# Performance work log

Measured on AMD Instinct MI355X. Metric: run time of the kernel, lower is better.

Reference implementation:

```python
import jax, jax.numpy as jnp
import numpy as np

INPUT_DIM = 1024
EMBED_DIM = 1024
NUM_HEADS = 16
HEAD_DIM = EMBED_DIM // NUM_HEADS


def _xavier_uniform(key, shape):
    fan_in, fan_out = shape[1], shape[0]
    limit = float(np.sqrt(6.0 / (fan_in + fan_out)))
    return jax.random.uniform(key, shape, jnp.float32, -limit, limit)


def setup_inputs() -> dict:
    key = jax.random.key(0)
    kx, kqkv, ko = jax.random.split(key, 3)
    x = jax.random.normal(kx, (2, 2048, INPUT_DIM), jnp.float32)
    # torch Linear stores weight as [out, in]; we keep that convention
    w_qkv = _xavier_uniform(kqkv, (3 * EMBED_DIM, INPUT_DIM))
    b_qkv = jnp.zeros((3 * EMBED_DIM,), jnp.float32)
    w_o = _xavier_uniform(ko, (EMBED_DIM, EMBED_DIM))
    b_o = jnp.zeros((EMBED_DIM,), jnp.float32)
    return {"x": x, "w_qkv": w_qkv, "b_qkv": b_qkv, "w_o": w_o, "b_o": b_o}


def reference(x, w_qkv, b_qkv, w_o, b_o):
    B, S, _ = x.shape
    H, D = NUM_HEADS, HEAD_DIM
    qkv = jnp.einsum("bsi,oi->bso", x, w_qkv) + b_qkv          # [B,S,3E]
    qkv = qkv.reshape(B, S, H, 3 * D).transpose(0, 2, 1, 3)    # [B,H,S,3D]
    q, k, v = jnp.split(qkv, 3, axis=-1)                        # each [B,H,S,D]
    scores = jnp.einsum("bhqd,bhkd->bhqk", q, k) / jnp.sqrt(jnp.float32(D))
    attn = jax.nn.softmax(scores, axis=-1)                      # [B,H,S,S]
    vals = jnp.einsum("bhqk,bhkd->bhqd", attn, v)               # [B,H,S,D]
    vals = vals.transpose(0, 2, 1, 3).reshape(B, S, H * D)      # [B,S,E]
    return jnp.einsum("bse,oe->bso", vals, w_o) + b_o
```

## Files before the change

### kernel.cpp

```cpp
#include <hip/hip_runtime.h>
#include <hip/hip_bf16.h>


typedef __attribute__((ext_vector_type(8))) short bf16x8;
typedef __attribute__((ext_vector_type(4))) short bf16x4;
typedef __attribute__((ext_vector_type(4))) float f32x4;

#define MFMA16(a, b, c) __builtin_amdgcn_mfma_f32_16x16x32_bf16((a), (b), (c), 0, 0, 0)

#if __has_builtin(__builtin_amdgcn_exp2f)
#define EXP2F(x) __builtin_amdgcn_exp2f(x)
#else
#define EXP2F(x) exp2f(x)
#endif

static __device__ __forceinline__ unsigned short f2bf_bits(float v) {
    __hip_bfloat16 h = __float2bfloat16(v);
    return *reinterpret_cast<unsigned short*>(&h);
}

static __device__ __forceinline__ bf16x8 cvt8(const float* p) {
    const f32x4 a = reinterpret_cast<const f32x4*>(p)[0];
    const f32x4 b = reinterpret_cast<const f32x4*>(p)[1];
    bf16x8 r;
    r[0] = (short)f2bf_bits(a[0]); r[1] = (short)f2bf_bits(a[1]);
    r[2] = (short)f2bf_bits(a[2]); r[3] = (short)f2bf_bits(a[3]);
    r[4] = (short)f2bf_bits(b[0]); r[5] = (short)f2bf_bits(b[1]);
    r[6] = (short)f2bf_bits(b[2]); r[7] = (short)f2bf_bits(b[3]);
    return r;
}

__device__ __forceinline__ bf16x8 ldg8(const __hip_bfloat16* p) {
    return *reinterpret_cast<const bf16x8*>(p);
}

__global__ __launch_bounds__(256)
void cast_f32_bf16(const float* __restrict__ src, __hip_bfloat16* __restrict__ dst) {
    const size_t base = ((size_t)blockIdx.x * 256 + threadIdx.x) * 32;
#pragma unroll
    for (int i = 0; i < 4; ++i)
        *reinterpret_cast<bf16x8*>(dst + base + i * 8) = cvt8(src + base + i * 8);
}

__global__ __launch_bounds__(256)
void qkv_gemm(const __hip_bfloat16* __restrict__ xb,
              const float* __restrict__ wqkv,
              const float* __restrict__ bqkv,
              __hip_bfloat16* __restrict__ Q,
              __hip_bfloat16* __restrict__ K,
              __hip_bfloat16* __restrict__ Vt) {
    __shared__ unsigned short As[128 * 40];
    __shared__ unsigned short Bs[128 * 40];

    const int tid  = threadIdx.x;
    const int lane = tid & 63;
    const int wv   = tid >> 6;
    const int quad = lane >> 4;
    const int l16  = lane & 15;
    const int wm   = wv >> 1;
    const int wn   = wv & 1;
    const int m0   = blockIdx.y * 128;
    const int n0   = blockIdx.x * 128;

    const int sr = tid >> 1;
    const int sc = (tid & 1) * 16;
    const __hip_bfloat16* ag = xb + (size_t)(m0 + sr) * 1024 + sc;
    const float*          bg = wqkv + (size_t)(n0 + sr) * 1024 + sc;
    unsigned short* aw = &As[sr * 40 + sc];
    unsigned short* bw = &Bs[sr * 40 + sc];

    f32x4 zv = {0.f, 0.f, 0.f, 0.f};
    f32x4 acc[4][4];
#pragma unroll
    for (int ii = 0; ii < 4; ++ii)
#pragma unroll
        for (int jj = 0; jj < 4; ++jj) acc[ii][jj] = zv;

    for (int k0 = 0; k0 < 1024; k0 += 32) {
        const bf16x8 av0 = ldg8(ag + k0), av1 = ldg8(ag + k0 + 8);
        const bf16x8 bv0 = cvt8(bg + k0), bv1 = cvt8(bg + k0 + 8);
        __syncthreads();
        reinterpret_cast<bf16x8*>(aw)[0] = av0;
        reinterpret_cast<bf16x8*>(aw)[1] = av1;
        reinterpret_cast<bf16x8*>(bw)[0] = bv0;
        reinterpret_cast<bf16x8*>(bw)[1] = bv1;
        __syncthreads();
        bf16x8 af[4], bf[4];
#pragma unroll
        for (int ii = 0; ii < 4; ++ii)
            af[ii] = *reinterpret_cast<const bf16x8*>(
                &As[(wm * 64 + ii * 16 + l16) * 40 + quad * 8]);
#pragma unroll
        for (int jj = 0; jj < 4; ++jj)
            bf[jj] = *reinterpret_cast<const bf16x8*>(
                &Bs[(wn * 64 + jj * 16 + l16) * 40 + quad * 8]);
#pragma unroll
        for (int ii = 0; ii < 4; ++ii)
#pragma unroll
            for (int jj = 0; jj < 4; ++jj)
                acc[ii][jj] = MFMA16(af[ii], bf[jj], acc[ii][jj]);
    }

    const float QSCALE = 0.18033688011f;

#pragma unroll
    for (int jj = 0; jj < 4; ++jj) {
        const int n = n0 + wn * 64 + jj * 16 + l16;
        const float bias = bqkv[n];
        const int h = n / 192;
        const int r = n - h * 192;
        const int t = r >> 6;
        const int d = r & 63;
#pragma unroll
        for (int ii = 0; ii < 4; ++ii) {
#pragma unroll
            for (int i = 0; i < 4; ++i) {
                const int m = m0 + wm * 64 + ii * 16 + quad * 4 + i;
                const int b = m >> 11;
                const int s = m & 2047;
                const int bh = b * 16 + h;
                float v = acc[ii][jj][i] + bias;
                if (t == 0) {
                    Q[((size_t)bh * 2048 + s) * 64 + d] = __float2bfloat16(v * QSCALE);
                } else if (t == 1) {
                    K[((size_t)bh * 2048 + s) * 64 + d] = __float2bfloat16(v);
                } else {
                    Vt[((size_t)bh * 64 + d) * 2048 + s] = __float2bfloat16(v);
                }
            }
        }
    }
}

__global__ __launch_bounds__(256)
void attn_kernel(const __hip_bfloat16* __restrict__ Q,
                 const __hip_bfloat16* __restrict__ K,
                 const __hip_bfloat16* __restrict__ Vt,
                 __hip_bfloat16* __restrict__ AO) {
    __shared__ unsigned short Ks0[32 * 40];
    __shared__ unsigned short Ks1[32 * 40];
    __shared__ unsigned short Vs[64 * 40];

    const int tid  = threadIdx.x;
    const int lane = tid & 63;
    const int wv   = tid >> 6;
    const int quad = lane >> 4;
    const int l16  = lane & 15;

    const int blk = blockIdx.x;
    const int xcd = blk & 7;
    const int sub = blk >> 3;
    const int bh  = xcd * 4 + (sub & 3);
    const int qb  = sub >> 2;
    const int q0  = qb * 128 + wv * 32;
    const int b   = bh >> 4;
    const int h   = bh & 15;

    const __hip_bfloat16* Qp = Q  + (size_t)bh * 131072;
    const __hip_bfloat16* Kp = K  + (size_t)bh * 131072;
    const __hip_bfloat16* Vp = Vt + (size_t)bh * 131072;

    bf16x8 bQ[2][2];
#pragma unroll
    for (int t = 0; t < 2; ++t)
#pragma unroll
        for (int dh = 0; dh < 2; ++dh)
            bQ[t][dh] = ldg8(Qp + (size_t)(q0 + t * 16 + l16) * 64 + dh * 32 + quad * 8);

    const int kr = tid >> 3;
    const int kc = (tid & 7) * 8;
    const int kb = kr & 7;
    const int sig = (kb < 4) ? ((kr >> 3) * 4 + kb) : (16 + (kr >> 3) * 4 + (kb - 4));
    unsigned short* kw = (kc < 32) ? &Ks0[sig * 40 + kc] : &Ks1[sig * 40 + (kc - 32)];
    const int vr = tid >> 2;
    const int vc = (tid & 3) * 8;
    unsigned short* vw = &Vs[vr * 40 + vc];

    f32x4 zv = {0.f, 0.f, 0.f, 0.f};
    f32x4 Of[2][4];
#pragma unroll
    for (int t = 0; t < 2; ++t)
#pragma unroll
        for (int jj = 0; jj < 4; ++jj) Of[t][jj] = zv;
    float li[2] = {0.f, 0.f};

    for (int kt = 0; kt < 64; ++kt) {
        const int key0 = kt * 32;

        const bf16x8 gk = ldg8(Kp + (size_t)(key0 + kr) * 64 + kc);
        const bf16x8 gv = ldg8(Vp + (size_t)vr * 2048 + key0 + vc);
        __syncthreads();
        *reinterpret_cast<bf16x8*>(kw) = gk;
        *reinterpret_cast<bf16x8*>(vw) = gv;
        __syncthreads();

        const bf16x8 aKA0 = *reinterpret_cast<const bf16x8*>(&Ks0[l16 * 40 + quad * 8]);
        const bf16x8 aKA1 = *reinterpret_cast<const bf16x8*>(&Ks1[l16 * 40 + quad * 8]);
        const bf16x8 aKB0 = *reinterpret_cast<const bf16x8*>(&Ks0[(16 + l16) * 40 + quad * 8]);
        const bf16x8 aKB1 = *reinterpret_cast<const bf16x8*>(&Ks1[(16 + l16) * 40 + quad * 8]);
        bf16x8 aV[4];
#pragma unroll
        for (int jj = 0; jj < 4; ++jj)
            aV[jj] = *reinterpret_cast<const bf16x8*>(&Vs[(jj * 16 + l16) * 40 + quad * 8]);

        f32x4 sA[2], sB[2];
#pragma unroll
        for (int t = 0; t < 2; ++t) {
            sA[t] = zv; sB[t] = zv;
            sA[t] = MFMA16(aKA0, bQ[t][0], sA[t]);
            sA[t] = MFMA16(aKA1, bQ[t][1], sA[t]);
            sB[t] = MFMA16(aKB0, bQ[t][0], sB[t]);
            sB[t] = MFMA16(aKB1, bQ[t][1], sB[t]);
        }

#pragma unroll
        for (int t = 0; t < 2; ++t) {
            float pA[4], pB[4];
#pragma unroll
            for (int i = 0; i < 4; ++i) {
                pA[i] = EXP2F(sA[t][i]);
                pB[i] = EXP2F(sB[t][i]);
            }
            li[t] += ((pA[0] + pA[1]) + (pA[2] + pA[3]))
                   + ((pB[0] + pB[1]) + (pB[2] + pB[3]));

            bf16x8 bP;
            bP[0] = (short)f2bf_bits(pA[0]); bP[1] = (short)f2bf_bits(pA[1]);
            bP[2] = (short)f2bf_bits(pA[2]); bP[3] = (short)f2bf_bits(pA[3]);
            bP[4] = (short)f2bf_bits(pB[0]); bP[5] = (short)f2bf_bits(pB[1]);
            bP[6] = (short)f2bf_bits(pB[2]); bP[7] = (short)f2bf_bits(pB[3]);

#pragma unroll
            for (int jj = 0; jj < 4; ++jj)
                Of[t][jj] = MFMA16(aV[jj], bP, Of[t][jj]);
        }
    }

#pragma unroll
    for (int t = 0; t < 2; ++t) {
        li[t] += __shfl_xor(li[t], 16);
        li[t] += __shfl_xor(li[t], 32);
    }

#pragma unroll
    for (int t = 0; t < 2; ++t) {
        const float linv = 1.f / li[t];
        const int s = q0 + t * 16 + l16;
        __hip_bfloat16* aop = AO + (((size_t)b * 2048 + s) * 16 + h) * 64;
#pragma unroll
        for (int jj = 0; jj < 4; ++jj) {
            bf16x4 pk;
#pragma unroll
            for (int i = 0; i < 4; ++i)
                pk[i] = (short)f2bf_bits(Of[t][jj][i] * linv);
            *reinterpret_cast<bf16x4*>(aop + jj * 16 + quad * 4) = pk;
        }
    }
}

__global__ __launch_bounds__(256)
void out_gemm(const __hip_bfloat16* __restrict__ A,
              const __hip_bfloat16* __restrict__ wob,
              const float* __restrict__ bo,
              float* __restrict__ out) {
    __shared__ unsigned short As[128 * 40];
    __shared__ unsigned short Bs[128 * 40];

    const int tid  = threadIdx.x;
    const int lane = tid & 63;
    const int wv   = tid >> 6;
    const int quad = lane >> 4;
    const int l16  = lane & 15;
    const int wm   = wv >> 1;
    const int wn   = wv & 1;
    const int m0   = blockIdx.y * 128;
    const int n0   = blockIdx.x * 128;

    const int sr = tid >> 1;
    const int sc = (tid & 1) * 16;
    const __hip_bfloat16* ag = A   + (size_t)(m0 + sr) * 1024 + sc;
    const __hip_bfloat16* bg = wob + (size_t)(n0 + sr) * 1024 + sc;
    unsigned short* aw = &As[sr * 40 + sc];
    unsigned short* bw = &Bs[sr * 40 + sc];

    f32x4 zv = {0.f, 0.f, 0.f, 0.f};
    f32x4 acc[4][4];
#pragma unroll
    for (int ii = 0; ii < 4; ++ii)
#pragma unroll
        for (int jj = 0; jj < 4; ++jj) acc[ii][jj] = zv;

    for (int k0 = 0; k0 < 1024; k0 += 32) {
        const bf16x8 av0 = ldg8(ag + k0), av1 = ldg8(ag + k0 + 8);
        const bf16x8 bv0 = ldg8(bg + k0), bv1 = ldg8(bg + k0 + 8);
        __syncthreads();
        reinterpret_cast<bf16x8*>(aw)[0] = av0;
        reinterpret_cast<bf16x8*>(aw)[1] = av1;
        reinterpret_cast<bf16x8*>(bw)[0] = bv0;
        reinterpret_cast<bf16x8*>(bw)[1] = bv1;
        __syncthreads();
        bf16x8 af[4], bf[4];
#pragma unroll
        for (int ii = 0; ii < 4; ++ii)
            af[ii] = *reinterpret_cast<const bf16x8*>(
                &As[(wm * 64 + ii * 16 + l16) * 40 + quad * 8]);
#pragma unroll
        for (int jj = 0; jj < 4; ++jj)
            bf[jj] = *reinterpret_cast<const bf16x8*>(
                &Bs[(wn * 64 + jj * 16 + l16) * 40 + quad * 8]);
#pragma unroll
        for (int ii = 0; ii < 4; ++ii)
#pragma unroll
            for (int jj = 0; jj < 4; ++jj)
                acc[ii][jj] = MFMA16(af[ii], bf[jj], acc[ii][jj]);
    }

#pragma unroll
    for (int jj = 0; jj < 4; ++jj) {
        const int n = n0 + wn * 64 + jj * 16 + l16;
        const float bias = bo[n];
#pragma unroll
        for (int ii = 0; ii < 4; ++ii) {
#pragma unroll
            for (int i = 0; i < 4; ++i) {
                const int m = m0 + wm * 64 + ii * 16 + quad * 4 + i;
                out[(size_t)m * 1024 + n] = acc[ii][jj][i] + bias;
            }
        }
    }
}

extern "C" void kernel_launch(void* const* d_in, const int* in_sizes, int n_in,
                              void* d_out, int out_size, void* d_ws, size_t ws_size,
                              hipStream_t stream) {
    const float* x    = (const float*)d_in[0];
    const float* wqkv = (const float*)d_in[1];
    const float* bqkv = (const float*)d_in[2];
    const float* wo   = (const float*)d_in[3];
    const float* bo   = (const float*)d_in[4];
    float* out = (float*)d_out;

    __hip_bfloat16* ws = (__hip_bfloat16*)d_ws;
    __hip_bfloat16* Q   = ws;
    __hip_bfloat16* K   = ws + (size_t)4194304;
    __hip_bfloat16* Vt  = ws + (size_t)8388608;
    __hip_bfloat16* AO  = ws + (size_t)12582912;
    __hip_bfloat16* xb  = AO;
    __hip_bfloat16* wob = Q;

    cast_f32_bf16<<<dim3(512), 256, 0, stream>>>(x, xb);
    qkv_gemm<<<dim3(24, 32), 256, 0, stream>>>(xb, wqkv, bqkv, Q, K, Vt);
    attn_kernel<<<dim3(512), 256, 0, stream>>>(Q, K, Vt, AO);
    cast_f32_bf16<<<dim3(128), 256, 0, stream>>>(wo, wob);
    out_gemm<<<dim3(8, 32), 256, 0, stream>>>(AO, wob, bo, out);
}
```

Baseline: 214.4 us.

## Pre-cast QKV weights to bf16 and remap GEMM blocks for XCD locality

Adds a separate cast kernel that converts w_qkv to bf16 once, staged in the output buffer, so the QKV GEMM loads bf16 weights instead of re-reading and converting fp32 tiles in every block. Both GEMMs switch to a 1D grid, and the QKV GEMM swizzles block ids so each XCD works on a contiguous group of N-tiles, aiming for better L2 reuse. This adds one kernel launch and a full pass over the weight matrix, and uses d_out as scratch space until out_gemm overwrites it.

Result: no change. 218.1 us (+1.7%).

```diff
diff --git a/kernel.cpp b/kernel.cpp
--- a/kernel.cpp
+++ b/kernel.cpp
@@ -44,7 +44,7 @@
 
 __global__ __launch_bounds__(256)
 void qkv_gemm(const __hip_bfloat16* __restrict__ xb,
-              const float* __restrict__ wqkv,
+              const __hip_bfloat16* __restrict__ wb,
               const float* __restrict__ bqkv,
               __hip_bfloat16* __restrict__ Q,
               __hip_bfloat16* __restrict__ K,
@@ -59,13 +59,17 @@
     const int l16  = lane & 15;
     const int wm   = wv >> 1;
     const int wn   = wv & 1;
-    const int m0   = blockIdx.y * 128;
-    const int n0   = blockIdx.x * 128;
+
+    const int bid = blockIdx.x;
+    const int xcd = bid & 7;
+    const int r   = bid >> 3;
+    const int m0  = (r / 3) * 128;
+    const int n0  = (xcd * 3 + (r % 3)) * 128;
 
     const int sr = tid >> 1;
     const int sc = (tid & 1) * 16;
     const __hip_bfloat16* ag = xb + (size_t)(m0 + sr) * 1024 + sc;
-    const float*          bg = wqkv + (size_t)(n0 + sr) * 1024 + sc;
+    const __hip_bfloat16* bg = wb + (size_t)(n0 + sr) * 1024 + sc;
     unsigned short* aw = &As[sr * 40 + sc];
     unsigned short* bw = &Bs[sr * 40 + sc];
 
@@ -78,7 +82,7 @@
 
     for (int k0 = 0; k0 < 1024; k0 += 32) {
         const bf16x8 av0 = ldg8(ag + k0), av1 = ldg8(ag + k0 + 8);
-        const bf16x8 bv0 = cvt8(bg + k0), bv1 = cvt8(bg + k0 + 8);
+        const bf16x8 bv0 = ldg8(bg + k0), bv1 = ldg8(bg + k0 + 8);
         __syncthreads();
         reinterpret_cast<bf16x8*>(aw)[0] = av0;
         reinterpret_cast<bf16x8*>(aw)[1] = av1;
@@ -108,9 +112,9 @@
         const int n = n0 + wn * 64 + jj * 16 + l16;
         const float bias = bqkv[n];
         const int h = n / 192;
-        const int r = n - h * 192;
-        const int t = r >> 6;
-        const int d = r & 63;
+        const int r2 = n - h * 192;
+        const int t = r2 >> 6;
+        const int d = r2 & 63;
 #pragma unroll
         for (int ii = 0; ii < 4; ++ii) {
 #pragma unroll
@@ -273,8 +277,10 @@
     const int l16  = lane & 15;
     const int wm   = wv >> 1;
     const int wn   = wv & 1;
-    const int m0   = blockIdx.y * 128;
-    const int n0   = blockIdx.x * 128;
+
+    const int bid = blockIdx.x;
+    const int m0  = (bid >> 3) * 128;
+    const int n0  = (bid & 7) * 128;
 
     const int sr = tid >> 1;
     const int sc = (tid & 1) * 16;
@@ -345,12 +351,15 @@
     __hip_bfloat16* K   = ws + (size_t)4194304;
     __hip_bfloat16* Vt  = ws + (size_t)8388608;
     __hip_bfloat16* AO  = ws + (size_t)12582912;
-    __hip_bfloat16* xb  = AO;
     __hip_bfloat16* wob = Q;
 
+    __hip_bfloat16* xb     = (__hip_bfloat16*)d_out;
+    __hip_bfloat16* wqkvb  = xb + (size_t)4194304;
+
     cast_f32_bf16<<<dim3(512), 256, 0, stream>>>(x, xb);
-    qkv_gemm<<<dim3(24, 32), 256, 0, stream>>>(xb, wqkv, bqkv, Q, K, Vt);
+    cast_f32_bf16<<<dim3(384), 256, 0, stream>>>(wqkv, wqkvb);
+    qkv_gemm<<<dim3(768), 256, 0, stream>>>(xb, wqkvb, bqkv, Q, K, Vt);
     attn_kernel<<<dim3(512), 256, 0, stream>>>(Q, K, Vt, AO);
     cast_f32_bf16<<<dim3(128), 256, 0, stream>>>(wo, wob);
-    out_gemm<<<dim3(8, 32), 256, 0, stream>>>(AO, wob, bo, out);
-}
+    out_gemm<<<dim3(256), 256, 0, stream>>>(AO, wob, bo, out);
+}
```
